# Kernel optimization log

Hardware: AMD Instinct MI355X
Metric: run time of the kernel (lower is better)

## Reference

```python
import jax, jax.numpy as jnp
import numpy as np

K = 3        # kernel size
PAD = 1      # padding
DG = 16      # deformable groups
MAXR = 10.0  # max_residue_magnitude


def _lrelu(x):
    return jnp.where(x >= 0, x, 0.1 * x)


def _conv3(x, w, b):
    y = jax.lax.conv_general_dilated(x, w, (1, 1), 'SAME',
                                     dimension_numbers=('NCHW', 'OIHW', 'NCHW'))
    return y + b[None, :, None, None]


def _deform_conv2d(x, offset, mask, weight, bias):
    # x: [B,Cin,H,W]; offset: [B,2*DG*K*K,H,W]; mask: [B,DG*K*K,H,W]
    B, Cin, H, W = x.shape
    Cout = weight.shape[0]
    G, Cg, K2 = DG, Cin // DG, K * K
    off = offset.reshape(B, G, K2, 2, H, W)
    dy, dx = off[:, :, :, 0], off[:, :, :, 1]
    ky = jnp.repeat(jnp.arange(K), K).astype(x.dtype)   # [K2]
    kx = jnp.tile(jnp.arange(K), K).astype(x.dtype)
    hh = jnp.arange(H, dtype=x.dtype)
    ww = jnp.arange(W, dtype=x.dtype)
    # sampling positions [B,G,K2,H,W]
    py = dy + ky[None, None, :, None, None] + hh[None, None, None, :, None] - PAD
    px = dx + kx[None, None, :, None, None] + ww[None, None, None, None, :] - PAD
    y0 = jnp.floor(py)
    x0 = jnp.floor(px)
    wy1 = py - y0
    wx1 = px - x0
    xf = x.reshape(B, G, Cg, H * W)

    def gather(yi, xi, wgt):
        valid = (yi >= 0) & (yi <= H - 1) & (xi >= 0) & (xi <= W - 1)
        idx = (jnp.clip(yi, 0, H - 1).astype(jnp.int32) * W
               + jnp.clip(xi, 0, W - 1).astype(jnp.int32)).reshape(B, G, -1)
        vals = jnp.take_along_axis(
            xf, jnp.broadcast_to(idx[:, :, None, :], (B, G, Cg, idx.shape[-1])), axis=3)
        vals = vals.reshape(B, G, Cg, K2, H, W)
        w = (wgt * valid.astype(x.dtype))[:, :, None]  # [B,G,1,K2,H,W]
        return vals * w

    s = (gather(y0, x0, (1 - wy1) * (1 - wx1))
         + gather(y0, x0 + 1, (1 - wy1) * wx1)
         + gather(y0 + 1, x0, wy1 * (1 - wx1))
         + gather(y0 + 1, x0 + 1, wy1 * wx1))
    s = s * mask.reshape(B, G, K2, H, W)[:, :, None]
    wr = weight.reshape(Cout, G, Cg, K2)
    out = jnp.einsum('ogck,bgckhw->bohw', wr, s)
    return out + bias[None, :, None, None]


def setup_inputs() -> dict:
    key = jax.random.key(0)
    ks = jax.random.split(key, 16)
    B, Cin, Cout, H, W = 4, 128, 64, 96, 96
    Coff = 3 * Cout + 4  # 196
    stdv = 1.0 / np.sqrt(Cin * K * K)
    inp = {
        'x': jax.random.normal(ks[0], (B, Cin, H, W), jnp.float32),
        'extra_feat': jax.random.normal(ks[1], (B, 3 * Cout, H, W), jnp.float32),
        'flow_1': jax.random.normal(ks[2], (B, 2, H, W), jnp.float32),
        'flow_2': jax.random.normal(ks[3], (B, 2, H, W), jnp.float32),
        'weight': jax.random.uniform(ks[4], (Cout, Cin, K, K), jnp.float32, -stdv, stdv),
        'bias': jax.random.normal(ks[5], (Cout,), jnp.float32) * 0.01,
        'ow0': jax.random.normal(ks[6], (Cout, Coff, K, K), jnp.float32) * 0.02,
        'ob0': jnp.zeros((Cout,), jnp.float32),
        'ow1': jax.random.normal(ks[7], (Cout, Cout, K, K), jnp.float32) * 0.02,
        'ob1': jnp.zeros((Cout,), jnp.float32),
        'ow2': jax.random.normal(ks[8], (Cout, Cout, K, K), jnp.float32) * 0.02,
        'ob2': jnp.zeros((Cout,), jnp.float32),
        'ow3': jax.random.normal(ks[9], (27 * DG, Cout, K, K), jnp.float32) * 0.01,
        'ob3': jnp.zeros((27 * DG,), jnp.float32),
    }
    return inp


def reference(x, extra_feat, flow_1, flow_2, weight, bias,
              ow0, ob0, ow1, ob1, ow2, ob2, ow3, ob3):
    feat = jnp.concatenate([extra_feat, flow_1, flow_2], axis=1)
    h = _lrelu(_conv3(feat, ow0, ob0))
    h = _lrelu(_conv3(h, ow1, ob1))
    h = _lrelu(_conv3(h, ow2, ob2))
    out = _conv3(h, ow3, ob3)
    o1, o2, m = jnp.split(out, 3, axis=1)
    offs = MAXR * jnp.tanh(jnp.concatenate([o1, o2], axis=1))
    off1, off2 = jnp.split(offs, 2, axis=1)
    off1 = off1 + jnp.tile(flow_1[:, ::-1], (1, off1.shape[1] // 2, 1, 1))
    off2 = off2 + jnp.tile(flow_2[:, ::-1], (1, off2.shape[1] // 2, 1, 1))
    offset = jnp.concatenate([off1, off2], axis=1)
    mask = jax.nn.sigmoid(m)
    return _deform_conv2d(x, offset, mask, weight, bias)
```

## Files before the change

### kernel.cpp

```cpp
#include <hip/hip_runtime.h>
#include <math.h>

#define HW 9216
#define Hh 96
#define Ww 96
#define PHW 9604

typedef __attribute__((ext_vector_type(8))) short bh8;
typedef __attribute__((ext_vector_type(4))) short bh4;
typedef __attribute__((ext_vector_type(4))) float f32x4;
typedef __attribute__((ext_vector_type(2))) float f32x2;
typedef __attribute__((ext_vector_type(4))) int i32x4;
union bh8i { bh8 v; i32x4 i; };

__device__ __forceinline__ short f2bf(float f) {
    union { float f; unsigned u; } v; v.f = f;
    unsigned r = v.u + 0x7FFFu + ((v.u >> 16) & 1u);
    return (short)(r >> 16);
}
__device__ __forceinline__ float bf2f(short s) {
    union { unsigned u; float f; } v; v.u = ((unsigned)(unsigned short)s) << 16;
    return v.f;
}
__device__ __forceinline__ float lo_bf(unsigned u) {
    union { unsigned u; float f; } v; v.u = u << 16; return v.f;
}
__device__ __forceinline__ float hi_bf(unsigned u) {
    union { unsigned u; float f; } v; v.u = u & 0xFFFF0000u; return v.f;
}
__device__ __forceinline__ unsigned pack_bf2(float lo, float hi) {
    union { float f; unsigned u; } a, b; a.f = lo; b.f = hi;
    unsigned ul = a.u + 0x7FFFu + ((a.u >> 16) & 1u);
    unsigned uh = b.u + 0x7FFFu + ((b.u >> 16) & 1u);
    return (ul >> 16) | (uh & 0xFFFF0000u);
}

__global__ void prep_misc(short* __restrict__ xpad1, short* __restrict__ hpa,
                          short* __restrict__ hpb, short* __restrict__ xdp,
                          const float* __restrict__ ow0, const float* __restrict__ ow1,
                          const float* __restrict__ ow2, const float* __restrict__ ow3,
                          const float* __restrict__ wd,
                          short* __restrict__ wb0, short* __restrict__ wb1,
                          short* __restrict__ wb2, short* __restrict__ wb3,
                          short* __restrict__ wbd) {
    int i = blockIdx.x * 256 + threadIdx.x;
    const int z1 = 4 * 388 * 224, z2 = 4 * 388 * 64;
    if (i < z1 + 2 * z2) {
        short* p; int C;
        if (i < z1) { p = xpad1; C = 224; }
        else if (i < z1 + z2) { p = hpa; C = 64; i -= z1; }
        else { p = hpb; C = 64; i -= z1 + z2; }
        int c = i % C;
        int r = i / C;
        int b = r / 388, pid = r - b * 388;
        int row, col;
        if (pid < 98)       { row = 0;  col = pid; }
        else if (pid < 196) { row = 97; col = pid - 98; }
        else if (pid < 292) { row = pid - 196 + 1; col = 0; }
        else                { row = pid - 292 + 1; col = 97; }
        p[((size_t)b * PHW + row * 98 + col) * C + c] = 0;
        return;
    }
    i -= z1 + 2 * z2;
    const int zr = 4 * 16 * 388 * 8;
    if (i < zr) {
        int c8 = i & 7;
        int r = i >> 3;
        int pid = r % 388;
        int bg = r / 388;
        int row, col;
        if (pid < 98)       { row = 0;  col = pid; }
        else if (pid < 196) { row = 97; col = pid - 98; }
        else if (pid < 292) { row = pid - 196 + 1; col = 0; }
        else                { row = pid - 292 + 1; col = 97; }
        xdp[((size_t)bg * PHW + row * 98 + col) * 8 + c8] = 0;
        return;
    }
    i -= zr;
    const int n0 = 64 * 9 * 224, n1 = 64 * 9 * 64, n3 = 448 * 9 * 64, nd = 64 * 1152;
    if (i < n0) {
        int co = i / (9 * 224); int r = i - co * (9 * 224);
        int tap = r / 224, ci = r - tap * 224;
        wb0[i] = f2bf(ci < 196 ? ow0[(co * 196 + ci) * 9 + tap] : 0.f);
        return;
    }
    i -= n0;
    if (i < n1) {
        int co = i / (9 * 64); int r = i - co * (9 * 64);
        int tap = r / 64, ci = r - tap * 64;
        wb1[i] = f2bf(ow1[(co * 64 + ci) * 9 + tap]);
        return;
    }
    i -= n1;
    if (i < n1) {
        int co = i / (9 * 64); int r = i - co * (9 * 64);
        int tap = r / 64, ci = r - tap * 64;
        wb2[i] = f2bf(ow2[(co * 64 + ci) * 9 + tap]);
        return;
    }
    i -= n1;
    if (i < n3) {
        int co = i / (9 * 64); int r = i - co * (9 * 64);
        int tap = r / 64, ci = r - tap * 64;
        wb3[i] = f2bf(co < 432 ? ow3[(co * 64 + ci) * 9 + tap] : 0.f);
        return;
    }
    i -= n3;
    if (i < nd) {
        int co = i / 1152, kd = i - co * 1152;
        int gt = kd >> 3, c = kd & 7;
        int g = gt / 9, tap = gt - g * 9;
        wbd[i] = f2bf(wd[(co * 128 + g * 8 + c) * 9 + tap]);
    }
}

__global__ void pack_all(const float* __restrict__ extra,
                         const float* __restrict__ f1,
                         const float* __restrict__ f2,
                         const float* __restrict__ x,
                         short* __restrict__ xp,
                         short* __restrict__ xdp) {
    __shared__ float t[32][33];
    const int tid = threadIdx.x, tx = tid & 31, ty = tid >> 5;
    const int pt = blockIdx.x, b = blockIdx.z;
    if (blockIdx.y < 7) {
        const int ct = blockIdx.y;
#pragma unroll
        for (int j = 0; j < 4; ++j) {
            int ch = ct * 32 + ty + j * 8;
            int p = pt * 32 + tx;
            float v = 0.f;
            if (ch < 192)      v = extra[(b * 192 + ch) * HW + p];
            else if (ch < 194) v = f1[(b * 2 + ch - 192) * HW + p];
            else if (ch < 196) v = f2[(b * 2 + ch - 194) * HW + p];
            t[ty + j * 8][tx] = v;
        }
        __syncthreads();
#pragma unroll
        for (int j = 0; j < 4; ++j) {
            int pr = ty + j * 8;
            int p = pt * 32 + pr;
            int r = p / 96, c = p - r * 96;
            xp[((size_t)b * PHW + (r + 1) * 98 + (c + 1)) * 224 + ct * 32 + tx] =
                f2bf(t[tx][pr]);
        }
    } else {
        const int ct = blockIdx.y - 7;
#pragma unroll
        for (int j = 0; j < 4; ++j) {
            int ch = ct * 32 + ty + j * 8;
            t[ty + j * 8][tx] = x[((size_t)b * 128 + ch) * HW + pt * 32 + tx];
        }
        __syncthreads();
        if (tid < 128) {
            int oct = tid >> 5, p = tid & 31;
            int g = ct * 4 + oct;
            int pix = pt * 32 + p;
            int r = pix / 96, c = pix - r * 96;
            bh8 v;
#pragma unroll
            for (int cc = 0; cc < 8; ++cc) v[cc] = f2bf(t[oct * 8 + cc][p]);
            *(bh8*)&xdp[(((size_t)b * 16 + g) * PHW + (r + 1) * 98 + (c + 1)) * 8] = v;
        }
    }
}

template<int CINP, int KCH>
__launch_bounds__(256)
__global__ void conv_mfma(const short* __restrict__ xp,
                          const short* __restrict__ wb,
                          const float* __restrict__ bias,
                          short* __restrict__ o1) {
    __shared__ __attribute__((aligned(16))) short smA[9 * 64 * 32];
    const int tid = threadIdx.x;
    const int lane = tid & 63, wv = tid >> 6;
    const int q = lane >> 4, l15 = lane & 15;
    const int b = blockIdx.y;
    const int pix0 = blockIdx.x * 64 + wv * 16;
    const int soh = pix0 / 96, sow = pix0 - (pix0 / 96) * 96;

    const short* bp = xp + ((size_t)b * PHW + soh * 98 + sow + l15) * CINP + q * 8;

    const int sco = tid >> 2, sqq = tid & 3;
    const short* wsrc = wb + (size_t)sco * (9 * CINP) + sqq * 8;

    f32x4 acc[4];
#pragma unroll
    for (int t = 0; t < 4; ++t) acc[t] = (f32x4){0.f, 0.f, 0.f, 0.f};

    for (int p = 0; p < KCH; ++p) {
        __syncthreads();
        bh8 wtmp[9];
#pragma unroll
        for (int tap = 0; tap < 9; ++tap)
            wtmp[tap] = *(const bh8*)(wsrc + tap * CINP + p * 32);
#pragma unroll
        for (int tap = 0; tap < 9; ++tap)
            *(bh8*)&smA[tap * 2048 + sco * 32 + sqq * 8] = wtmp[tap];
        __syncthreads();
#pragma unroll
        for (int tap = 0; tap < 9; ++tap) {
            const int ky = tap / 3, kx = tap - (tap / 3) * 3;
            bh8 bf = *(const bh8*)(bp + (ky * 98 + kx) * CINP + p * 32);
#pragma unroll
            for (int t = 0; t < 4; ++t) {
                bh8 af = *(const bh8*)&smA[tap * 2048 + (t * 16 + l15) * 32 + q * 8];
                acc[t] = __builtin_amdgcn_mfma_f32_16x16x32_bf16(af, bf, acc[t], 0, 0, 0);
            }
        }
    }

    size_t base = ((size_t)b * PHW + (soh + 1) * 98 + sow + l15 + 1) * 64;
#pragma unroll
    for (int t = 0; t < 4; ++t) {
        bh4 v4;
#pragma unroll
        for (int r = 0; r < 4; ++r) {
            int co = t * 16 + q * 4 + r;
            float v = acc[t][r] + bias[co];
            v = (v >= 0.f) ? v : 0.1f * v;
            v4[r] = f2bf(v);
        }
        *(bh4*)(o1 + base + t * 16 + q * 4) = v4;
    }
}

__launch_bounds__(256)
__global__ void conv4_gemm(const short* __restrict__ xp,
                           const short* __restrict__ wb,
                           const float* __restrict__ bias,
                           float* __restrict__ offp,
                           short* __restrict__ maskb,
                           const float* __restrict__ flow1,
                           const float* __restrict__ flow2) {
    __shared__ __attribute__((aligned(16))) short smA[64 * 64];
    const int tid = threadIdx.x;
    const int lane = tid & 63, wv = tid >> 6;
    const int q = lane >> 4, l15 = lane & 15;
    const int b = blockIdx.y;
    const int cob = blockIdx.z * 64;
    const int pixw = blockIdx.x * 192 + wv * 48;

    const short* bp[3];
#pragma unroll
    for (int s = 0; s < 3; ++s) {
        int pixs = pixw + s * 16;
        int soh = pixs / 96, sow = pixs - (pixs / 96) * 96;
        bp[s] = xp + ((size_t)b * PHW + soh * 98 + sow + l15) * 64 + q * 8;
    }

    f32x4 acc[4][3];
#pragma unroll
    for (int cf = 0; cf < 4; ++cf)
#pragma unroll
        for (int s = 0; s < 3; ++s) acc[cf][s] = (f32x4){0.f, 0.f, 0.f, 0.f};

    for (int tap = 0; tap < 9; ++tap) {
        const int ky = tap / 3, kx = tap - (tap / 3) * 3;
        __syncthreads();
#pragma unroll
        for (int it = 0; it < 2; ++it) {
            int id = it * 256 + tid;
            int row = id >> 3, s = id & 7;
            int sw = s ^ (row & 7);
            *(bh8*)&smA[row * 64 + sw * 8] =
                *(const bh8*)(wb + (size_t)(cob + row) * 576 + tap * 64 + s * 8);
        }
        __syncthreads();
#pragma unroll
        for (int kc = 0; kc < 2; ++kc) {
            bh8 bf[3], af[4];
#pragma unroll
            for (int s = 0; s < 3; ++s)
                bf[s] = *(const bh8*)(bp[s] + (ky * 98 + kx) * 64 + kc * 32);
#pragma unroll
            for (int cf = 0; cf < 4; ++cf) {
                int row = cf * 16 + l15;
                int sw = (kc * 4 + q) ^ (row & 7);
                af[cf] = *(const bh8*)&smA[row * 64 + sw * 8];
            }
#pragma unroll
            for (int cf = 0; cf < 4; ++cf)
#pragma unroll
                for (int s = 0; s < 3; ++s)
                    acc[cf][s] = __builtin_amdgcn_mfma_f32_16x16x32_bf16(
                        af[cf], bf[s], acc[cf][s], 0, 0, 0);
        }
    }

#pragma unroll
    for (int s = 0; s < 3; ++s) {
        int pix = pixw + s * 16 + l15;
#pragma unroll
        for (int cf = 0; cf < 4; ++cf) {
            int cb0 = cob + cf * 16 + q * 4;
            if (cb0 < 288) {
                const float* fl = (cb0 < 144) ? flow1 : flow2;
                float fe = fl[(b * 2 + 1) * HW + pix];
                float fo = fl[(b * 2) * HW + pix];
                float t0 = 10.f * tanhf(acc[cf][s][0] + bias[cb0 + 0]) + fe;
                float t1 = 10.f * tanhf(acc[cf][s][1] + bias[cb0 + 1]) + fo;
                float t2 = 10.f * tanhf(acc[cf][s][2] + bias[cb0 + 2]) + fe;
                float t3 = 10.f * tanhf(acc[cf][s][3] + bias[cb0 + 3]) + fo;
                size_t p0 = ((size_t)b * 144 + (cb0 >> 1)) * HW + pix;
                *(f32x2*)&offp[p0 * 2] = (f32x2){t0, t1};
                *(f32x2*)&offp[(p0 + HW) * 2] = (f32x2){t2, t3};
            } else {
#pragma unroll
                for (int r = 0; r < 4; ++r) {
                    int chn = cb0 + r;
                    if (chn < 432) {
                        float v = acc[cf][s][r] + bias[chn];
                        maskb[((size_t)b * 144 + (chn - 288)) * HW + pix] =
                            f2bf(1.f / (1.f + expf(-v)));
                    }
                }
            }
        }
    }
}

__launch_bounds__(256)
__global__ void deform_mfma(const short* __restrict__ xdp,
                            const float* __restrict__ offp,
                            const short* __restrict__ maskb,
                            const short* __restrict__ wbd,
                            const float* __restrict__ bias,
                            float* __restrict__ out) {
    __shared__ float red[4][1024];
    const int tid = threadIdx.x;
    const int lane = tid & 63, wv = tid >> 6;
    const int q = lane >> 4, l15 = lane & 15;
    const int blk = blockIdx.x;
    const int xs = blk & 7, idx = blk >> 3;
    const int b = xs >> 1;
    const int pix0 = ((xs & 1) * 288 + idx) * 16;
    const int pix = pix0 + l15;
    const int h = pix / 96, w = pix - (pix / 96) * 96;

    const float* opp = offp + ((size_t)b * 144 * HW + pix) * 2;
    const short* mp = maskb + (size_t)b * 144 * HW + pix;
    const short* xb = xdp + (size_t)b * 16 * PHW * 8;
    const short* ap = wbd + (size_t)l15 * 1152 + wv * 288 + q * 8;

    f32x2 dxy[9];
    float mk[9];
#pragma unroll
    for (int i = 0; i < 9; ++i) {
        const int gt = wv * 36 + i * 4 + q;
        dxy[i] = *(const f32x2*)(opp + (size_t)gt * HW * 2);
        mk[i] = bf2f(mp[(size_t)gt * HW]);
    }

    const short* cp[9];
    f32x4 ww[9];
#pragma unroll
    for (int i = 0; i < 9; ++i) {
        const int gt = wv * 36 + i * 4 + q;
        const int g = gt / 9, tap = gt - (gt / 9) * 9;
        float py = dxy[i][0] + (float)(tap / 3) + (float)h - 1.f;
        float px = dxy[i][1] + (float)(tap - (tap / 3) * 3) + (float)w - 1.f;
        py = fminf(fmaxf(py, -1.f), 96.f);
        px = fminf(fmaxf(px, -1.f), 96.f);
        float y0f = floorf(py), x0f = floorf(px);
        float wy1 = py - y0f, wx1 = px - x0f;
        float wy0 = 1.f - wy1, wx0 = 1.f - wx1;
        int yp = (int)y0f + 1, xp = (int)x0f + 1;
        cp[i] = xb + ((size_t)g * PHW + yp * 98 + xp) * 8;
        float m = mk[i];
        ww[i] = (f32x4){wy0 * wx0 * m, wy0 * wx1 * m, wy1 * wx0 * m, wy1 * wx1 * m};
    }

    f32x4 acc[4];
#pragma unroll
    for (int t = 0; t < 4; ++t) acc[t] = (f32x4){0.f, 0.f, 0.f, 0.f};

#pragma unroll
    for (int i = 0; i < 9; ++i) {
        bh8i c00, c01, c10, c11;
        c00.v = *(const bh8*)(cp[i]);
        c01.v = *(const bh8*)(cp[i] + 8);
        c10.v = *(const bh8*)(cp[i] + 98 * 8);
        c11.v = *(const bh8*)(cp[i] + 99 * 8);
        const float w00 = ww[i][0], w01 = ww[i][1], w10 = ww[i][2], w11 = ww[i][3];
        bh8i bf;
#pragma unroll
        for (int k = 0; k < 4; ++k) {
            unsigned u00 = (unsigned)c00.i[k], u01 = (unsigned)c01.i[k];
            unsigned u10 = (unsigned)c10.i[k], u11 = (unsigned)c11.i[k];
            float lo = w00 * lo_bf(u00) + w01 * lo_bf(u01)
                     + w10 * lo_bf(u10) + w11 * lo_bf(u11);
            float hi = w00 * hi_bf(u00) + w01 * hi_bf(u01)
                     + w10 * hi_bf(u10) + w11 * hi_bf(u11);
            bf.i[k] = (int)pack_bf2(lo, hi);
        }
#pragma unroll
        for (int t = 0; t < 4; ++t) {
            bh8 af = *(const bh8*)(ap + (size_t)t * 16 * 1152 + i * 32);
            acc[t] = __builtin_amdgcn_mfma_f32_16x16x32_bf16(af, bf.v, acc[t], 0, 0, 0);
        }
    }

#pragma unroll
    for (int t = 0; t < 4; ++t)
#pragma unroll
        for (int r = 0; r < 4; ++r)
            red[wv][(t * 16 + q * 4 + r) * 16 + l15] = acc[t][r];
    __syncthreads();
    for (int e = tid; e < 1024; e += 256) {
        int co = e >> 4, pl = e & 15;
        float v = red[0][e] + red[1][e] + red[2][e] + red[3][e] + bias[co];
        out[((size_t)b * 64 + co) * HW + pix0 + pl] = v;
    }
}

extern "C" void kernel_launch(void* const* d_in, const int* in_sizes, int n_in,
                              void* d_out, int out_size, void* d_ws, size_t ws_size,
                              hipStream_t stream) {
    const float* x      = (const float*)d_in[0];
    const float* extra  = (const float*)d_in[1];
    const float* flow1  = (const float*)d_in[2];
    const float* flow2  = (const float*)d_in[3];
    const float* weight = (const float*)d_in[4];
    const float* bias   = (const float*)d_in[5];
    const float* ow0    = (const float*)d_in[6];
    const float* ob0    = (const float*)d_in[7];
    const float* ow1    = (const float*)d_in[8];
    const float* ob1    = (const float*)d_in[9];
    const float* ow2    = (const float*)d_in[10];
    const float* ob2    = (const float*)d_in[11];
    const float* ow3    = (const float*)d_in[12];
    const float* ob3    = (const float*)d_in[13];
    float* out = (float*)d_out;

    char* wsb = (char*)d_ws;
    short* xpad1 = (short*)wsb;   wsb += (size_t)4 * PHW * 224 * 2;
    short* hpa   = (short*)wsb;   wsb += (size_t)4 * PHW * 64 * 2;
    short* hpb   = (short*)wsb;   wsb += (size_t)4 * PHW * 64 * 2;
    float* offpair = (float*)wsb; wsb += (size_t)4 * 144 * HW * 2 * 4;
    short* maskbuf = (short*)wsb; wsb += (size_t)4 * 144 * HW * 2;
    short* xdp     = (short*)wsb; wsb += (size_t)4 * 16 * PHW * 8 * 2 + 32;
    short* wb0     = (short*)wsb; wsb += 64 * 9 * 224 * 2;
    short* wb1     = (short*)wsb; wsb += 64 * 9 * 64 * 2;
    short* wb2     = (short*)wsb; wsb += 64 * 9 * 64 * 2;
    short* wb3     = (short*)wsb; wsb += 448 * 9 * 64 * 2;
    short* wbd     = (short*)wsb;

    const int prep_total = 546304 + 198656 + 534528;
    prep_misc<<<dim3((prep_total + 255) / 256), 256, 0, stream>>>(
        xpad1, hpa, hpb, xdp, ow0, ow1, ow2, ow3, weight,
        wb0, wb1, wb2, wb3, wbd);
    pack_all<<<dim3(288, 11, 4), 256, 0, stream>>>(extra, flow1, flow2, x, xpad1, xdp);

    conv_mfma<224, 7><<<dim3(144, 4), 256, 0, stream>>>(xpad1, wb0, ob0, hpa);
    conv_mfma<64, 2><<<dim3(144, 4), 256, 0, stream>>>(hpa, wb1, ob1, hpb);
    conv_mfma<64, 2><<<dim3(144, 4), 256, 0, stream>>>(hpb, wb2, ob2, hpa);
    conv4_gemm<<<dim3(48, 4, 7), 256, 0, stream>>>(hpa, wb3, ob3, offpair,
                                                   maskbuf, flow1, flow2);
    deform_mfma<<<dim3(2304), 256, 0, stream>>>(xdp, offpair, maskbuf, wbd, bias, out);
}
```

Measured before the change: 313.8 us.

## Preload full conv4 weight slice into LDS once and widen per-wave pixel tile

The conv4 GEMM kernel now loads all 18 K-chunks of its 64-row weight slice into shared memory once, instead of reloading one tap per iteration between two barriers. The per-iteration syncthreads are gone. Each wave now covers 64 pixels (4 subtiles) instead of 48, so the grid shrinks from 48 to 36 blocks in x. The cost is 72KB of LDS per block, which limits occupancy, and more accumulator registers; the swizzle was dropped, so LDS reads may hit bank conflicts.

```diff
diff --git a/kernel.cpp b/kernel.cpp
--- a/kernel.cpp
+++ b/kernel.cpp
@@ -233,64 +233,61 @@
                            short* __restrict__ maskb,
                            const float* __restrict__ flow1,
                            const float* __restrict__ flow2) {
-    __shared__ __attribute__((aligned(16))) short smA[64 * 64];
+    __shared__ __attribute__((aligned(16))) short smA[18 * 64 * 32];
     const int tid = threadIdx.x;
     const int lane = tid & 63, wv = tid >> 6;
     const int q = lane >> 4, l15 = lane & 15;
     const int b = blockIdx.y;
     const int cob = blockIdx.z * 64;
-    const int pixw = blockIdx.x * 192 + wv * 48;
-
-    const short* bp[3];
-#pragma unroll
-    for (int s = 0; s < 3; ++s) {
-        int pixs = pixw + s * 16;
+    const int pix0 = blockIdx.x * 256 + wv * 64;
+
+    {
+        const int row = tid >> 2, s = tid & 3;
+        const short* asrc = wb + (size_t)(cob + row) * 576 + s * 8;
+#pragma unroll
+        for (int c = 0; c < 18; ++c) {
+            *(bh8*)&smA[c * 2048 + row * 32 + s * 8] = *(const bh8*)(asrc + c * 32);
+        }
+    }
+
+    const short* bp[4];
+#pragma unroll
+    for (int s = 0; s < 4; ++s) {
+        int pixs = pix0 + s * 16;
         int soh = pixs / 96, sow = pixs - (pixs / 96) * 96;
         bp[s] = xp + ((size_t)b * PHW + soh * 98 + sow + l15) * 64 + q * 8;
     }
 
-    f32x4 acc[4][3];
+    f32x4 acc[4][4];
 #pragma unroll
     for (int cf = 0; cf < 4; ++cf)
 #pragma unroll
-        for (int s = 0; s < 3; ++s) acc[cf][s] = (f32x4){0.f, 0.f, 0.f, 0.f};
-
-    for (int tap = 0; tap < 9; ++tap) {
+        for (int s = 0; s < 4; ++s) acc[cf][s] = (f32x4){0.f, 0.f, 0.f, 0.f};
+
+    __syncthreads();
+
+#pragma unroll 2
+    for (int ch = 0; ch < 18; ++ch) {
+        const int tap = ch >> 1, kc = ch & 1;
         const int ky = tap / 3, kx = tap - (tap / 3) * 3;
-        __syncthreads();
-#pragma unroll
-        for (int it = 0; it < 2; ++it) {
-            int id = it * 256 + tid;
-            int row = id >> 3, s = id & 7;
-            int sw = s ^ (row & 7);
-            *(bh8*)&smA[row * 64 + sw * 8] =
-                *(const bh8*)(wb + (size_t)(cob + row) * 576 + tap * 64 + s * 8);
-        }
-        __syncthreads();
-#pragma unroll
-        for (int kc = 0; kc < 2; ++kc) {
-            bh8 bf[3], af[4];
-#pragma unroll
-            for (int s = 0; s < 3; ++s)
-                bf[s] = *(const bh8*)(bp[s] + (ky * 98 + kx) * 64 + kc * 32);
-#pragma unroll
-            for (int cf = 0; cf < 4; ++cf) {
-                int row = cf * 16 + l15;
-                int sw = (kc * 4 + q) ^ (row & 7);
-                af[cf] = *(const bh8*)&smA[row * 64 + sw * 8];
-            }
-#pragma unroll
-            for (int cf = 0; cf < 4; ++cf)
-#pragma unroll
-                for (int s = 0; s < 3; ++s)
-                    acc[cf][s] = __builtin_amdgcn_mfma_f32_16x16x32_bf16(
-                        af[cf], bf[s], acc[cf][s], 0, 0, 0);
-        }
-    }
-
-#pragma unroll
-    for (int s = 0; s < 3; ++s) {
-        int pix = pixw + s * 16 + l15;
+        bh8 bf[4], af[4];
+#pragma unroll
+        for (int s = 0; s < 4; ++s)
+            bf[s] = *(const bh8*)(bp[s] + (ky * 98 + kx) * 64 + kc * 32);
+#pragma unroll
+        for (int cf = 0; cf < 4; ++cf)
+            af[cf] = *(const bh8*)&smA[ch * 2048 + (cf * 16 + l15) * 32 + q * 8];
+#pragma unroll
+        for (int cf = 0; cf < 4; ++cf)
+#pragma unroll
+            for (int s = 0; s < 4; ++s)
+                acc[cf][s] = __builtin_amdgcn_mfma_f32_16x16x32_bf16(
+                    af[cf], bf[s], acc[cf][s], 0, 0, 0);
+    }
+
+#pragma unroll
+    for (int s = 0; s < 4; ++s) {
+        int pix = pix0 + s * 16 + l15;
 #pragma unroll
         for (int cf = 0; cf < 4; ++cf) {
             int cb0 = cob + cf * 16 + q * 4;
@@ -455,7 +452,7 @@
     conv_mfma<224, 7><<<dim3(144, 4), 256, 0, stream>>>(xpad1, wb0, ob0, hpa);
     conv_mfma<64, 2><<<dim3(144, 4), 256, 0, stream>>>(hpa, wb1, ob1, hpb);
     conv_mfma<64, 2><<<dim3(144, 4), 256, 0, stream>>>(hpb, wb2, ob2, hpa);
-    conv4_gemm<<<dim3(48, 4, 7), 256, 0, stream>>>(hpa, wb3, ob3, offpair,
+    conv4_gemm<<<dim3(36, 4, 7), 256, 0, stream>>>(hpa, wb3, ob3, offpair,
                                                    maskbuf, flow1, flow2);
     deform_mfma<<<dim3(2304), 256, 0, stream>>>(xdp, offpair, maskbuf, wbd, bias, out);
 }
```

After: 324.8 us. 1.03x slower.

## Stage conv4 weights via async global-to-LDS loads in three-tap phases

Applied to the files above, without the earlier changes.

conv4_gemm now loads the weight tile with global_load_lds, writing directly into shared memory. Each stage covers three taps and both K-chunks, so the loop has 3 barrier pairs instead of 9, and the XOR swizzle is replaced by a plain 32-wide row layout. Launch bounds with a minimum of 2 blocks per SM are added to conv4_gemm and deform_mfma, which may limit registers. The unswizzled LDS layout could cause bank conflicts, and the 24KB shared buffer may reduce occupancy.

```diff
diff --git a/kernel.cpp b/kernel.cpp
--- a/kernel.cpp
+++ b/kernel.cpp
@@ -33,6 +33,13 @@
     unsigned ul = a.u + 0x7FFFu + ((a.u >> 16) & 1u);
     unsigned uh = b.u + 0x7FFFu + ((b.u >> 16) & 1u);
     return (ul >> 16) | (uh & 0xFFFF0000u);
+}
+
+__device__ __forceinline__ void async_lds16(const short* g, short* l) {
+    __builtin_amdgcn_global_load_lds(
+        (const __attribute__((address_space(1))) unsigned int*)g,
+        (__attribute__((address_space(3))) unsigned int*)l,
+        16, 0, 0);
 }
 
 __global__ void prep_misc(short* __restrict__ xpad1, short* __restrict__ hpa,
@@ -225,7 +232,7 @@
     }
 }
 
-__launch_bounds__(256)
+__launch_bounds__(256, 2)
 __global__ void conv4_gemm(const short* __restrict__ xp,
                            const short* __restrict__ wb,
                            const float* __restrict__ bias,
@@ -233,7 +240,7 @@
                            short* __restrict__ maskb,
                            const float* __restrict__ flow1,
                            const float* __restrict__ flow2) {
-    __shared__ __attribute__((aligned(16))) short smA[64 * 64];
+    __shared__ __attribute__((aligned(16))) short smA[6 * 64 * 32];
     const int tid = threadIdx.x;
     const int lane = tid & 63, wv = tid >> 6;
     const int q = lane >> 4, l15 = lane & 15;
@@ -249,36 +256,35 @@
         bp[s] = xp + ((size_t)b * PHW + soh * 98 + sow + l15) * 64 + q * 8;
     }
 
+    const short* asrc = wb + (size_t)(cob + wv * 16 + (lane >> 2)) * 576 + (lane & 3) * 8;
+    short* sdst = &smA[wv * 512];
+
     f32x4 acc[4][3];
 #pragma unroll
     for (int cf = 0; cf < 4; ++cf)
 #pragma unroll
         for (int s = 0; s < 3; ++s) acc[cf][s] = (f32x4){0.f, 0.f, 0.f, 0.f};
 
-    for (int tap = 0; tap < 9; ++tap) {
-        const int ky = tap / 3, kx = tap - (tap / 3) * 3;
-        __syncthreads();
-#pragma unroll
-        for (int it = 0; it < 2; ++it) {
-            int id = it * 256 + tid;
-            int row = id >> 3, s = id & 7;
-            int sw = s ^ (row & 7);
-            *(bh8*)&smA[row * 64 + sw * 8] =
-                *(const bh8*)(wb + (size_t)(cob + row) * 576 + tap * 64 + s * 8);
-        }
-        __syncthreads();
-#pragma unroll
-        for (int kc = 0; kc < 2; ++kc) {
+#pragma unroll
+    for (int ph = 0; ph < 3; ++ph) {
+        __syncthreads();
+#pragma unroll
+        for (int c6 = 0; c6 < 6; ++c6) {
+            const int tap = ph * 3 + (c6 >> 1), kc = c6 & 1;
+            async_lds16(asrc + tap * 64 + kc * 32, sdst + c6 * 2048);
+        }
+        __syncthreads();
+#pragma unroll
+        for (int c6 = 0; c6 < 6; ++c6) {
+            const int tap = ph * 3 + (c6 >> 1), kc = c6 & 1;
+            const int ky = tap / 3, kx = tap - (tap / 3) * 3;
             bh8 bf[3], af[4];
 #pragma unroll
             for (int s = 0; s < 3; ++s)
                 bf[s] = *(const bh8*)(bp[s] + (ky * 98 + kx) * 64 + kc * 32);
 #pragma unroll
-            for (int cf = 0; cf < 4; ++cf) {
-                int row = cf * 16 + l15;
-                int sw = (kc * 4 + q) ^ (row & 7);
-                af[cf] = *(const bh8*)&smA[row * 64 + sw * 8];
-            }
+            for (int cf = 0; cf < 4; ++cf)
+                af[cf] = *(const bh8*)&smA[c6 * 2048 + (cf * 16 + l15) * 32 + q * 8];
 #pragma unroll
             for (int cf = 0; cf < 4; ++cf)
 #pragma unroll
@@ -320,7 +326,7 @@
     }
 }
 
-__launch_bounds__(256)
+__launch_bounds__(256, 2)
 __global__ void deform_mfma(const short* __restrict__ xdp,
                             const float* __restrict__ offp,
                             const short* __restrict__ maskb,
```

Result: no change. 314.5 us (+0.2%).
